# Kernel optimization log

Hardware: AMD Instinct MI355X
Metric: run time of the kernel (lower is better)

## Reference

```python
import jax, jax.numpy as jnp
import numpy as np

D_MODEL = 1024
N_HEADS = 16
D_HEAD = D_MODEL // N_HEADS


def _pid_proj(x, Wp, Wi, Wd, Wg, bg):
    # x: (B, T, D). PID decomposition: proportional / integral (running mean) / derivative (diff).
    T = x.shape[1]
    denom = jnp.arange(1, T + 1, dtype=x.dtype)[None, :, None]
    integral = jnp.cumsum(x, axis=1) / denom
    derivative = jnp.concatenate([jnp.zeros_like(x[:, :1]), x[:, 1:] - x[:, :-1]], axis=1)
    g = jax.nn.softmax(x @ Wg.T + bg, axis=-1)  # (B, T, 3)
    return (g[..., 0:1] * (x @ Wp.T)
            + g[..., 1:2] * (integral @ Wi.T)
            + g[..., 2:3] * (derivative @ Wd.T))


def setup_inputs() -> dict:
    key = jax.random.key(0)
    ks = jax.random.split(key, 16)
    B, T, D = 2, 2048, D_MODEL
    s = 1.0 / np.sqrt(D)

    def lin(k):
        return jax.random.uniform(k, (D, D), jnp.float32, -s, s)

    inp = {"x": jax.random.normal(ks[0], (B, T, D), jnp.float32)}
    names = ["q", "k", "v"]
    i = 1
    for n in names:
        inp[n + "Wp"] = lin(ks[i]); i += 1
        inp[n + "Wi"] = lin(ks[i]) * 0.1; i += 1
        inp[n + "Wd"] = lin(ks[i]) * 0.1; i += 1
        inp[n + "Wg"] = jax.random.uniform(ks[i], (3, D), jnp.float32, -s, s); i += 1
        inp[n + "bg"] = jnp.array([1.0, 0.0, 0.0], jnp.float32)
    inp["oW"] = lin(ks[i]); i += 1
    inp["ob"] = jax.random.uniform(ks[i], (D,), jnp.float32, -s, s)
    return inp


def reference(x, qWp, qWi, qWd, qWg, qbg,
              kWp, kWi, kWd, kWg, kbg,
              vWp, vWi, vWd, vWg, vbg, oW, ob):
    B, T, D = x.shape
    H, dh = N_HEADS, D_HEAD
    Q = _pid_proj(x, qWp, qWi, qWd, qWg, qbg).reshape(B, T, H, dh).transpose(0, 2, 1, 3)
    K = _pid_proj(x, kWp, kWi, kWd, kWg, kbg).reshape(B, T, H, dh).transpose(0, 2, 1, 3)
    V = _pid_proj(x, vWp, vWi, vWd, vWg, vbg).reshape(B, T, H, dh).transpose(0, 2, 1, 3)
    scale = jnp.sqrt(jnp.asarray(dh, x.dtype))
    scores = jnp.einsum('bhqd,bhkd->bhqk', Q, K) / scale  # (B,H,T,T)
    causal = jnp.triu(jnp.ones((T, T), bool), k=1)
    scores = jnp.where(causal[None, None], -jnp.inf, scores)
    attn = jax.nn.softmax(scores, axis=-1)
    out = jnp.einsum('bhqk,bhkd->bhqd', attn, V)
    out = out.transpose(0, 2, 1, 3).reshape(B, T, D)
    return out @ oW.T + ob
```

## Files before the change

kernel.cpp:

```cpp
#include <hip/hip_runtime.h>
#include <hip/hip_bf16.h>


#define D_MODEL 1024
#define T_SEQ   2048
#define B_SZ    2
#define M_ROWS  (B_SZ * T_SEQ)
#define N_HEADS 16
#define D_HEAD  64

typedef unsigned short u16;
typedef unsigned int   u32;

typedef short  short8  __attribute__((ext_vector_type(8)));
typedef float  float4v __attribute__((ext_vector_type(4)));

__device__ __forceinline__ float bf2f(u16 u) {
    union { u32 i; float f; } c; c.i = ((u32)u) << 16; return c.f;
}
__device__ __forceinline__ u16 f2bf(float f) {
    union { float f; u32 i; } c; c.f = f;
    u32 i = c.i;
    i += 0x7FFFu + ((i >> 16) & 1u);
    return (u16)(i >> 16);
}
__device__ __forceinline__ u16 f2bfc(float f) {
    __hip_bfloat16 h = __float2bfloat16(f);
    union { __hip_bfloat16 h; u16 u; } c; c.h = h; return c.u;
}
__device__ __forceinline__ float ldin(const void* p, int i, int fl) {
    return fl ? ((const float*)p)[i] : bf2f(((const u16*)p)[i]);
}

__global__ void detect_kernel(const u32* __restrict__ x, int* __restrict__ flag)
{
    if (threadIdx.x == 0 && blockIdx.x == 0) {
        int good = 0;
        for (int i = 0; i < 256; ++i) {
            union { u32 u; float f; } c; c.u = x[i];
            float a = fabsf(c.f);
            if (c.f == c.f && a > 1e-8f && a < 1e4f) ++good;
        }
        *flag = (good >= 192) ? 1 : 0;
    }
}

__global__ __launch_bounds__(256) void scan_partial(
    const void* __restrict__ x, float* __restrict__ csum,
    const int* __restrict__ flagp)
{
    int fl = *flagp;
    int tid = blockIdx.x * 256 + threadIdx.x;
    int b = tid >> 14;
    int c = (tid >> 10) & 15;
    int d = tid & 1023;
    int base = (b * T_SEQ + c * 128) * D_MODEL + d;
    float s = 0.f;
#pragma unroll 8
    for (int t = 0; t < 128; ++t) s += ldin(x, base + t * D_MODEL, fl);
    csum[tid] = s;
}

__global__ __launch_bounds__(256) void scan_final(
    const void* __restrict__ x, const float* __restrict__ csum,
    u16* __restrict__ integ, u16* __restrict__ db,
    const int* __restrict__ flagp)
{
    int fl = *flagp;
    int tid = blockIdx.x * 256 + threadIdx.x;
    int b = tid >> 14;
    int c = (tid >> 10) & 15;
    int d = tid & 1023;
    float pre = 0.f;
    int cbase = (b << 14) | d;
    for (int cc = 0; cc < c; ++cc) pre += csum[cbase + (cc << 10)];
    int base = (b * T_SEQ + c * 128) * D_MODEL + d;
    float run = pre;
    int t0 = c * 128;
    float xprev = (c != 0) ? ldin(x, base - D_MODEL, fl) : 0.f;
    for (int t = 0; t < 128; ++t) {
        float xv = ldin(x, base + t * D_MODEL, fl);
        run += xv;
        integ[base + t * D_MODEL] = f2bf(run / (float)(t0 + t + 1));
        float dv = (t0 + t == 0) ? 0.f : (xv - xprev);
        db[base + t * D_MODEL] = f2bf(dv);
        xprev = xv;
    }
}

__global__ __launch_bounds__(64) void gates_kernel(
    const void* __restrict__ x,
    const void* __restrict__ qWg, const void* __restrict__ qbg,
    const void* __restrict__ kWg, const void* __restrict__ kbg,
    const void* __restrict__ vWg, const void* __restrict__ vbg,
    float* __restrict__ gq, float* __restrict__ gk, float* __restrict__ gv,
    const int* __restrict__ flagp)
{
    int fl = *flagp;
    int row = blockIdx.x;
    int l = threadIdx.x;
    int xb = row * D_MODEL;
    float p[9];
#pragma unroll
    for (int j = 0; j < 9; ++j) p[j] = 0.f;
#pragma unroll 4
    for (int i = 0; i < 16; ++i) {
        int d = l + 64 * i;
        float xv = ldin(x, xb + d, fl);
        p[0] += xv * ldin(qWg, d, fl);
        p[1] += xv * ldin(qWg, 1024 + d, fl);
        p[2] += xv * ldin(qWg, 2048 + d, fl);
        p[3] += xv * ldin(kWg, d, fl);
        p[4] += xv * ldin(kWg, 1024 + d, fl);
        p[5] += xv * ldin(kWg, 2048 + d, fl);
        p[6] += xv * ldin(vWg, d, fl);
        p[7] += xv * ldin(vWg, 1024 + d, fl);
        p[8] += xv * ldin(vWg, 2048 + d, fl);
    }
#pragma unroll
    for (int off = 32; off > 0; off >>= 1) {
#pragma unroll
        for (int j = 0; j < 9; ++j) p[j] += __shfl_down(p[j], off);
    }
    if (l == 0) {
        const void* bgs[3] = { qbg, kbg, vbg };
        float* outs[3] = { gq, gk, gv };
#pragma unroll
        for (int pr = 0; pr < 3; ++pr) {
            float a0 = p[pr * 3 + 0] + ldin(bgs[pr], 0, fl);
            float a1 = p[pr * 3 + 1] + ldin(bgs[pr], 1, fl);
            float a2 = p[pr * 3 + 2] + ldin(bgs[pr], 2, fl);
            float mx = fmaxf(a0, fmaxf(a1, a2));
            float e0 = __expf(a0 - mx), e1 = __expf(a1 - mx), e2 = __expf(a2 - mx);
            float inv = 1.f / (e0 + e1 + e2);
            outs[pr][row * 3 + 0] = e0 * inv;
            outs[pr][row * 3 + 1] = e1 * inv;
            outs[pr][row * 3 + 2] = e2 * inv;
        }
    }
}

struct CvtArgs { const void* src[10]; };

__global__ __launch_bounds__(256) void cvt_w(
    CvtArgs a, u16* __restrict__ dst, const int* __restrict__ flagp)
{
    int fl = *flagp;
    int m = blockIdx.y;
    u16* d = dst + ((size_t)m << 20);
    int i = (blockIdx.x * 256 + threadIdx.x) * 8;
    if (fl) {
        const float* s = (const float*)a.src[m];
        float4 v0 = *(const float4*)(s + i);
        float4 v1 = *(const float4*)(s + i + 4);
        ushort4 o0, o1;
        o0.x = f2bfc(v0.x); o0.y = f2bfc(v0.y); o0.z = f2bfc(v0.z); o0.w = f2bfc(v0.w);
        o1.x = f2bfc(v1.x); o1.y = f2bfc(v1.y); o1.z = f2bfc(v1.z); o1.w = f2bfc(v1.w);
        *(ushort4*)(d + i) = o0;
        *(ushort4*)(d + i + 4) = o1;
    } else {
        const u16* s = (const u16*)a.src[m];
        *(ushort4*)(d + i)     = *(const ushort4*)(s + i);
        *(ushort4*)(d + i + 4) = *(const ushort4*)(s + i + 4);
    }
}

struct GemmArgs {
    const void* W[3][3];
    const float* G[3];
    u16* C[3];
};

template<int MODE, int BW16>
__global__ __launch_bounds__(256, 3) void mfma_gemm(
    const void* __restrict__ X, const u16* __restrict__ Ib,
    const u16* __restrict__ Abf, GemmArgs args,
    const void* __restrict__ bias, void* __restrict__ outp,
    const int* __restrict__ flagp, int Ktot)
{
    int fl = *flagp;
    __shared__ __align__(16) u16 As[2 * 4096];
    __shared__ __align__(16) u16 Bs[2 * 4096];

    int tid = threadIdx.x;
    int l = tid & 63, w = tid >> 6;
    int wm = w >> 1, wn = w & 1;
    int lin = blockIdx.x + (blockIdx.y << 3);
    int m0 = ((((lin & 7) << 2) + (lin >> 6))) * 128;
    int n0 = ((lin >> 3) & 7) * 128;
    int z = blockIdx.z;
    int lane15 = l & 15, quad = l >> 4;
    int srow = tid >> 2;
    int cs = tid & 3;
    int skof = cs * 8;

    const void* W0; const void* W1; const void* W2;
    const float* G = nullptr;
    u16* Chead = nullptr;
    if (MODE == 0) {
        W0 = args.W[z][0]; W1 = args.W[z][1]; W2 = args.W[z][2];
        G = args.G[z]; Chead = args.C[z];
    } else {
        W0 = args.W[0][0]; W1 = W0; W2 = W0;
    }

    float gcoef[2][3];
    if (MODE == 0) {
#pragma unroll
        for (int c = 0; c < 2; ++c)
#pragma unroll
            for (int s = 0; s < 3; ++s)
                gcoef[c][s] = G[(m0 + c * 64 + srow) * 3 + s];
    }

    ushort4 ra[2][2];
    ushort4 rb[2][2];

    auto cvt4 = [](float4 t) {
        ushort4 u;
        u.x = f2bfc(t.x); u.y = f2bfc(t.y); u.z = f2bfc(t.z); u.w = f2bfc(t.w);
        return u;
    };
    auto ld8 = [&](const void* p, int idx, ushort4& o0, ushort4& o1) {
        if (fl) {
            o0 = cvt4(*(const float4*)((const float*)p + idx));
            o1 = cvt4(*(const float4*)((const float*)p + idx + 4));
        } else {
            o0 = *(const ushort4*)((const u16*)p + idx);
            o1 = *(const ushort4*)((const u16*)p + idx + 4);
        }
    };

    auto load_phase = [&](int k0) {
        int seg = k0 >> 10, ksrc = k0 & 1023;
        const void* Wse = (MODE == 0) ? (seg == 0 ? W0 : (seg == 1 ? W1 : W2)) : W0;
#pragma unroll
        for (int c = 0; c < 2; ++c) {
            int gm = m0 + c * 64 + srow;
            int idx = gm * 1024 + ksrc + skof;
            if (MODE == 1) {
                ra[c][0] = *(const ushort4*)&Abf[idx];
                ra[c][1] = *(const ushort4*)&Abf[idx + 4];
            } else if (seg == 1) {
                ra[c][0] = *(const ushort4*)&Ib[idx];
                ra[c][1] = *(const ushort4*)&Ib[idx + 4];
            } else if (seg == 2) {
                ra[c][0] = *(const ushort4*)&Abf[idx];
                ra[c][1] = *(const ushort4*)&Abf[idx + 4];
            } else {
                ld8(X, idx, ra[c][0], ra[c][1]);
            }
            int gn = n0 + c * 64 + srow;
            int bidx = gn * 1024 + ksrc + skof;
            if (BW16) {
                const u16* bs = (const u16*)Wse;
                rb[c][0] = *(const ushort4*)&bs[bidx];
                rb[c][1] = *(const ushort4*)&bs[bidx + 4];
            } else {
                ld8(Wse, bidx, rb[c][0], rb[c][1]);
            }
        }
    };

    auto unp8 = [](ushort4 a, ushort4 b, float v[8]) {
        v[0] = bf2f(a.x); v[1] = bf2f(a.y); v[2] = bf2f(a.z); v[3] = bf2f(a.w);
        v[4] = bf2f(b.x); v[5] = bf2f(b.y); v[6] = bf2f(b.z); v[7] = bf2f(b.w);
    };

    int wo[2];
#pragma unroll
    for (int c = 0; c < 2; ++c) {
        int g = c * 16 + ((srow >> 4) << 2) + cs;
        wo[c] = (g << 7) | ((((srow & 15) + g) & 15) << 3);
    }

    auto store_phase = [&](int k0, int buf) {
        int seg = k0 >> 10;
        u16* Ad = As + buf * 4096;
        u16* Bd = Bs + buf * 4096;
#pragma unroll
        for (int c = 0; c < 2; ++c) {
            short8 pk;
            if (MODE == 1) {
                pk[0] = (short)ra[c][0].x; pk[1] = (short)ra[c][0].y;
                pk[2] = (short)ra[c][0].z; pk[3] = (short)ra[c][0].w;
                pk[4] = (short)ra[c][1].x; pk[5] = (short)ra[c][1].y;
                pk[6] = (short)ra[c][1].z; pk[7] = (short)ra[c][1].w;
            } else {
                float v[8];
                unp8(ra[c][0], ra[c][1], v);
                float sc = gcoef[c][seg];
#pragma unroll
                for (int j = 0; j < 8; ++j) pk[j] = (short)f2bfc(v[j] * sc);
            }
            *(short8*)&Ad[wo[c]] = pk;

            short8 pb;
            pb[0] = (short)rb[c][0].x; pb[1] = (short)rb[c][0].y;
            pb[2] = (short)rb[c][0].z; pb[3] = (short)rb[c][0].w;
            pb[4] = (short)rb[c][1].x; pb[5] = (short)rb[c][1].y;
            pb[6] = (short)rb[c][1].z; pb[7] = (short)rb[c][1].w;
            *(short8*)&Bd[wo[c]] = pb;
        }
    };

    float4v acc[4][4];
#pragma unroll
    for (int i = 0; i < 4; ++i)
#pragma unroll
        for (int j = 0; j < 4; ++j)
#pragma unroll
            for (int r = 0; r < 4; ++r) acc[i][j][r] = 0.f;

    int aro[4], bro[4];
#pragma unroll
    for (int t = 0; t < 4; ++t) {
        int ga = (wm * 4 + t) * 4 + quad;
        aro[t] = (ga << 7) | (((lane15 + ga) & 15) << 3);
        int gb = (wn * 4 + t) * 4 + quad;
        bro[t] = (gb << 7) | (((lane15 + gb) & 15) << 3);
    }

    int nIt = Ktot >> 5;
    load_phase(0);
    store_phase(0, 0);

    for (int it = 0; it < nIt; ++it) {
        __syncthreads();
        int cur = it & 1;
        if (it + 1 < nIt) load_phase((it + 1) << 5);

        short8 af[4], bfr[4];
#pragma unroll
        for (int ms = 0; ms < 4; ++ms)
            af[ms] = *(const short8*)&As[cur * 4096 + aro[ms]];
#pragma unroll
        for (int ns = 0; ns < 4; ++ns)
            bfr[ns] = *(const short8*)&Bs[cur * 4096 + bro[ns]];
#pragma unroll
        for (int ms = 0; ms < 4; ++ms)
#pragma unroll
            for (int ns = 0; ns < 4; ++ns)
                acc[ms][ns] = __builtin_amdgcn_mfma_f32_16x16x32_bf16(
                    af[ms], bfr[ns], acc[ms][ns], 0, 0, 0);

        if (it + 1 < nIt) store_phase((it + 1) << 5, 1 - cur);
    }

#pragma unroll
    for (int ms = 0; ms < 4; ++ms) {
#pragma unroll
        for (int r = 0; r < 4; ++r) {
            int m = m0 + wm * 64 + ms * 16 + quad * 4 + r;
#pragma unroll
            for (int ns = 0; ns < 4; ++ns) {
                int n = n0 + wn * 64 + ns * 16 + lane15;
                float vv = acc[ms][ns][r];
                if (MODE == 0) {
                    int b = m >> 11, t = m & (T_SEQ - 1);
                    int h = n >> 6,  d = n & 63;
                    Chead[(((b << 4) + h) * T_SEQ + t) * 64 + d] = f2bf(vv);
                } else {
                    vv += ldin(bias, n, fl);
                    if (fl) ((float*)outp)[m * 1024 + n] = vv;
                    else    ((u16*)outp)[m * 1024 + n] = f2bf(vv);
                }
            }
        }
    }
}

__global__ __launch_bounds__(256) void attn_mfma(
    const u16* __restrict__ Qh, const u16* __restrict__ Kh,
    const u16* __restrict__ Vh, u16* __restrict__ AO)
{
    int bx = blockIdx.x;
    int i  = bx & 31;
    int qt = (i & 1) ? (31 - (i >> 1)) : (i >> 1);
    int bh = bx >> 5;
    int h  = bh & 15;
    int b  = bh >> 4;
    int tid = threadIdx.x;
    int l   = tid & 63;
    int w   = tid >> 6;
    int lane15 = l & 15;
    int quad   = l >> 4;

    __shared__ __align__(16) u16 Ks[64 * 72];
    __shared__ __align__(16) u16 Vt[64 * 72];
    __shared__ __align__(16) u16 Ps[4 * 16 * 72];

    const u16* Qb = Qh + bh * (T_SEQ * 64);
    const u16* Kb = Kh + bh * (T_SEQ * 64);
    const u16* Vb = Vh + bh * (T_SEQ * 64);

    int qrow = qt * 64 + w * 16 + lane15;
    short8 qf[2];
#pragma unroll
    for (int ks = 0; ks < 2; ++ks)
        qf[ks] = *(const short8*)&Qb[qrow * 64 + ks * 32 + quad * 8];

    float4v oacc[4];
#pragma unroll
    for (int ds = 0; ds < 4; ++ds)
#pragma unroll
        for (int r = 0; r < 4; ++r) oacc[ds][r] = 0.f;
    float mrun[4], lrun[4];
#pragma unroll
    for (int r = 0; r < 4; ++r) { mrun[r] = -1e30f; lrun[r] = 0.f; }

    int srow = tid >> 2;
    int sdc  = (tid & 3) * 16;

    short8 kr0, kr1, vr0, vr1;
    auto load_regs = [&](int kt) {
        const u16* kp = &Kb[(kt * 64 + srow) * 64 + sdc];
        kr0 = *(const short8*)kp;
        kr1 = *(const short8*)(kp + 8);
        const u16* vp = &Vb[(kt * 64 + srow) * 64 + sdc];
        vr0 = *(const short8*)vp;
        vr1 = *(const short8*)(vp + 8);
    };
    auto store_lds = [&]() {
        *(short8*)&Ks[srow * 72 + sdc] = kr0;
        *(short8*)&Ks[srow * 72 + sdc + 8] = kr1;
        u16 vv[16];
        *(short8*)&vv[0] = vr0;
        *(short8*)&vv[8] = vr1;
#pragma unroll
        for (int e2 = 0; e2 < 16; ++e2)
            Vt[(sdc + e2) * 72 + srow] = vv[e2];
    };

    load_regs(0);

    for (int kt = 0; kt <= qt; ++kt) {
        store_lds();
        __syncthreads();
        if (kt < qt) load_regs(kt + 1);

        float4v sacc[4];
#pragma unroll
        for (int ns = 0; ns < 4; ++ns)
#pragma unroll
            for (int r = 0; r < 4; ++r) sacc[ns][r] = 0.f;
#pragma unroll
        for (int ks = 0; ks < 2; ++ks) {
#pragma unroll
            for (int ns = 0; ns < 4; ++ns) {
                short8 bfk = *(const short8*)&Ks[(ns * 16 + lane15) * 72 + ks * 32 + quad * 8];
                sacc[ns] = __builtin_amdgcn_mfma_f32_16x16x32_bf16(
                    qf[ks], bfk, sacc[ns], 0, 0, 0);
            }
        }

        if (kt == qt) {
            int qg0 = qt * 64 + w * 16 + quad * 4;
#pragma unroll
            for (int ns = 0; ns < 4; ++ns) {
                int kg = kt * 64 + ns * 16 + lane15;
#pragma unroll
                for (int r = 0; r < 4; ++r) {
                    float s = sacc[ns][r] * 0.125f;
                    sacc[ns][r] = (kg > qg0 + r) ? -1e30f : s;
                }
            }
        } else {
#pragma unroll
            for (int ns = 0; ns < 4; ++ns)
#pragma unroll
                for (int r = 0; r < 4; ++r)
                    sacc[ns][r] *= 0.125f;
        }

#pragma unroll
        for (int r = 0; r < 4; ++r) {
            float mx = fmaxf(fmaxf(sacc[0][r], sacc[1][r]),
                             fmaxf(sacc[2][r], sacc[3][r]));
#pragma unroll
            for (int m2 = 1; m2 < 16; m2 <<= 1)
                mx = fmaxf(mx, __shfl_xor(mx, m2, 64));
            float mnew = fmaxf(mrun[r], mx);
            float al = __expf(mrun[r] - mnew);
            float rs = 0.f;
#pragma unroll
            for (int ns = 0; ns < 4; ++ns) {
                float p = __expf(sacc[ns][r] - mnew);
                sacc[ns][r] = p;
                rs += p;
            }
#pragma unroll
            for (int m2 = 1; m2 < 16; m2 <<= 1)
                rs += __shfl_xor(rs, m2, 64);
            lrun[r] = lrun[r] * al + rs;
            mrun[r] = mnew;
#pragma unroll
            for (int ds = 0; ds < 4; ++ds) oacc[ds][r] *= al;
        }

        u16* Pw = &Ps[w * 16 * 72];
#pragma unroll
        for (int ns = 0; ns < 4; ++ns)
#pragma unroll
            for (int r = 0; r < 4; ++r)
                Pw[(quad * 4 + r) * 72 + ns * 16 + lane15] = f2bf(sacc[ns][r]);

#pragma unroll
        for (int ks = 0; ks < 2; ++ks) {
            short8 afp = *(const short8*)&Pw[lane15 * 72 + ks * 32 + quad * 8];
#pragma unroll
            for (int ds = 0; ds < 4; ++ds) {
                short8 bfv = *(const short8*)&Vt[(ds * 16 + lane15) * 72 + ks * 32 + quad * 8];
                oacc[ds] = __builtin_amdgcn_mfma_f32_16x16x32_bf16(
                    afp, bfv, oacc[ds], 0, 0, 0);
            }
        }
        __syncthreads();
    }

#pragma unroll
    for (int r = 0; r < 4; ++r) {
        float inv = 1.f / lrun[r];
        int t = qt * 64 + w * 16 + quad * 4 + r;
        int orow = (b * T_SEQ + t) * 1024 + h * 64;
#pragma unroll
        for (int ds = 0; ds < 4; ++ds)
            AO[orow + ds * 16 + lane15] = f2bf(oacc[ds][r] * inv);
    }
}

extern "C" void kernel_launch(void* const* d_in, const int* in_sizes, int n_in,
                              void* d_out, int out_size, void* d_ws, size_t ws_size,
                              hipStream_t stream)
{
    const void* x   = d_in[0];
    const void* qWp = d_in[1];
    const void* qWi = d_in[2];
    const void* qWd = d_in[3];
    const void* qWg = d_in[4];
    const void* qbg = d_in[5];
    const void* kWp = d_in[6];
    const void* kWi = d_in[7];
    const void* kWd = d_in[8];
    const void* kWg = d_in[9];
    const void* kbg = d_in[10];
    const void* vWp = d_in[11];
    const void* vWi = d_in[12];
    const void* vWd = d_in[13];
    const void* vWg = d_in[14];
    const void* vbg = d_in[15];
    const void* oW  = d_in[16];
    const void* ob  = d_in[17];

    const size_t SZ = (size_t)M_ROWS * D_MODEL;

    int*   flag = (int*)d_ws;
    float* fws  = (float*)d_ws;
    float* csum = fws + 64;
    float* gq   = csum + 32768;
    float* gk   = gq + 3 * M_ROWS;
    float* gv   = gk + 3 * M_ROWS;
    u16* Ib = (u16*)((char*)d_ws + (1u << 20));
    u16* AO = Ib;
    u16* Qh = Ib + SZ;
    u16* Kh = Qh + SZ;
    u16* Vh = Kh + SZ;

    u16* db = (u16*)d_out;

    const size_t NEED_FULL = (size_t)(1u << 20) + 4 * SZ * 2 + ((size_t)10 << 21);
    u16* wb = (ws_size >= NEED_FULL) ? (Vh + SZ) : nullptr;

    detect_kernel<<<1, 64, 0, stream>>>((const u32*)x, flag);
    scan_partial<<<128, 256, 0, stream>>>(x, csum, flag);
    scan_final<<<128, 256, 0, stream>>>(x, csum, Ib, db, flag);
    gates_kernel<<<M_ROWS, 64, 0, stream>>>(x, qWg, qbg, kWg, kbg, vWg, vbg,
                                            gq, gk, gv, flag);

    GemmArgs pa;
    pa.G[0] = gq; pa.G[1] = gk; pa.G[2] = gv;
    pa.C[0] = Qh; pa.C[1] = Kh; pa.C[2] = Vh;
    GemmArgs oa = {};

    if (wb) {
        CvtArgs ca;
        ca.src[0] = qWp; ca.src[1] = qWi; ca.src[2] = qWd;
        ca.src[3] = kWp; ca.src[4] = kWi; ca.src[5] = kWd;
        ca.src[6] = vWp; ca.src[7] = vWi; ca.src[8] = vWd;
        ca.src[9] = oW;
        cvt_w<<<dim3(512, 10), 256, 0, stream>>>(ca, wb, flag);

        for (int z2 = 0; z2 < 3; ++z2)
            for (int s2 = 0; s2 < 3; ++s2)
                pa.W[z2][s2] = wb + ((size_t)(z2 * 3 + s2) << 20);
        oa.W[0][0] = wb + ((size_t)9 << 20);

        mfma_gemm<0, 1><<<dim3(8, 32, 3), 256, 0, stream>>>(
            x, Ib, db, pa, nullptr, nullptr, flag, 3072);
        attn_mfma<<<B_SZ * N_HEADS * (T_SEQ / 64), 256, 0, stream>>>(Qh, Kh, Vh, AO);
        mfma_gemm<1, 1><<<dim3(8, 32, 1), 256, 0, stream>>>(
            nullptr, nullptr, AO, oa, ob, d_out, flag, 1024);
    } else {
        pa.W[0][0] = qWp; pa.W[0][1] = qWi; pa.W[0][2] = qWd;
        pa.W[1][0] = kWp; pa.W[1][1] = kWi; pa.W[1][2] = kWd;
        pa.W[2][0] = vWp; pa.W[2][1] = vWi; pa.W[2][2] = vWd;
        oa.W[0][0] = oW;

        mfma_gemm<0, 0><<<dim3(8, 32, 3), 256, 0, stream>>>(
            x, Ib, db, pa, nullptr, nullptr, flag, 3072);
        attn_mfma<<<B_SZ * N_HEADS * (T_SEQ / 64), 256, 0, stream>>>(Qh, Kh, Vh, AO);
        mfma_gemm<1, 0><<<dim3(8, 32, 1), 256, 0, stream>>>(
            nullptr, nullptr, AO, oa, ob, d_out, flag, 1024);
    }
}
```

Baseline: 494.0 us.

## Split-K the output projection with atomics and double scan chunk count

The output projection GEMM is split along K into two halves. Each half atomically adds into an fp32 accumulator that is zeroed first, and a separate kernel then adds the bias and writes the output, doubling the block count on a grid that previously had only 256 blocks. The prefix-scan kernels now use 64-row chunks instead of 128-row chunks, giving twice as many threads and a shorter serial loop per thread. This adds a memset, atomic traffic and an extra launch in exchange for better CU occupancy.

```diff
diff --git a/kernel.cpp b/kernel.cpp
--- a/kernel.cpp
+++ b/kernel.cpp
@@ -51,13 +51,13 @@
 {
     int fl = *flagp;
     int tid = blockIdx.x * 256 + threadIdx.x;
-    int b = tid >> 14;
-    int c = (tid >> 10) & 15;
+    int b = tid >> 15;
+    int c = (tid >> 10) & 31;
     int d = tid & 1023;
-    int base = (b * T_SEQ + c * 128) * D_MODEL + d;
+    int base = (b * T_SEQ + c * 64) * D_MODEL + d;
     float s = 0.f;
 #pragma unroll 8
-    for (int t = 0; t < 128; ++t) s += ldin(x, base + t * D_MODEL, fl);
+    for (int t = 0; t < 64; ++t) s += ldin(x, base + t * D_MODEL, fl);
     csum[tid] = s;
 }
 
@@ -68,17 +68,17 @@
 {
     int fl = *flagp;
     int tid = blockIdx.x * 256 + threadIdx.x;
-    int b = tid >> 14;
-    int c = (tid >> 10) & 15;
+    int b = tid >> 15;
+    int c = (tid >> 10) & 31;
     int d = tid & 1023;
     float pre = 0.f;
-    int cbase = (b << 14) | d;
+    int cbase = (b << 15) | d;
     for (int cc = 0; cc < c; ++cc) pre += csum[cbase + (cc << 10)];
-    int base = (b * T_SEQ + c * 128) * D_MODEL + d;
+    int base = (b * T_SEQ + c * 64) * D_MODEL + d;
     float run = pre;
-    int t0 = c * 128;
+    int t0 = c * 64;
     float xprev = (c != 0) ? ldin(x, base - D_MODEL, fl) : 0.f;
-    for (int t = 0; t < 128; ++t) {
+    for (int t = 0; t < 64; ++t) {
         float xv = ldin(x, base + t * D_MODEL, fl);
         run += xv;
         integ[base + t * D_MODEL] = f2bf(run / (float)(t0 + t + 1));
@@ -165,13 +165,34 @@
     }
 }
 
+__global__ __launch_bounds__(256) void finish_o(
+    const float* __restrict__ acc32, const void* __restrict__ bias,
+    void* __restrict__ outp, const int* __restrict__ flagp)
+{
+    int fl = *flagp;
+    int i4 = (blockIdx.x * 256 + threadIdx.x) * 4;
+    float4 v = *(const float4*)(acc32 + i4);
+    int n = i4 & 1023;
+    v.x += ldin(bias, n + 0, fl);
+    v.y += ldin(bias, n + 1, fl);
+    v.z += ldin(bias, n + 2, fl);
+    v.w += ldin(bias, n + 3, fl);
+    if (fl) {
+        *(float4*)((float*)outp + i4) = v;
+    } else {
+        ushort4 o;
+        o.x = f2bfc(v.x); o.y = f2bfc(v.y); o.z = f2bfc(v.z); o.w = f2bfc(v.w);
+        *(ushort4*)((u16*)outp + i4) = o;
+    }
+}
+
 struct GemmArgs {
     const void* W[3][3];
     const float* G[3];
     u16* C[3];
 };
 
-template<int MODE, int BW16>
+template<int MODE, int BW16, int SPLIT>
 __global__ __launch_bounds__(256, 3) void mfma_gemm(
     const void* __restrict__ X, const u16* __restrict__ Ib,
     const u16* __restrict__ Abf, GemmArgs args,
@@ -189,6 +210,7 @@
     int m0 = ((((lin & 7) << 2) + (lin >> 6))) * 128;
     int n0 = ((lin >> 3) & 7) * 128;
     int z = blockIdx.z;
+    int kbase = (MODE == 1 && SPLIT) ? (z << 9) : 0;
     int lane15 = l & 15, quad = l >> 4;
     int srow = tid >> 2;
     int cs = tid & 3;
@@ -232,7 +254,7 @@
     };
 
     auto load_phase = [&](int k0) {
-        int seg = k0 >> 10, ksrc = k0 & 1023;
+        int seg = k0 >> 10, ksrc = (k0 & 1023) + kbase;
         const void* Wse = (MODE == 0) ? (seg == 0 ? W0 : (seg == 1 ? W1 : W2)) : W0;
 #pragma unroll
         for (int c = 0; c < 2; ++c) {
@@ -360,6 +382,8 @@
                     int b = m >> 11, t = m & (T_SEQ - 1);
                     int h = n >> 6,  d = n & 63;
                     Chead[(((b << 4) + h) * T_SEQ + t) * 64 + d] = f2bf(vv);
+                } else if (SPLIT) {
+                    atomicAdd(&((float*)outp)[m * 1024 + n], vv);
                 } else {
                     vv += ldin(bias, n, fl);
                     if (fl) ((float*)outp)[m * 1024 + n] = vv;
@@ -557,7 +581,7 @@
     int*   flag = (int*)d_ws;
     float* fws  = (float*)d_ws;
     float* csum = fws + 64;
-    float* gq   = csum + 32768;
+    float* gq   = csum + 65536;
     float* gk   = gq + 3 * M_ROWS;
     float* gv   = gk + 3 * M_ROWS;
     u16* Ib = (u16*)((char*)d_ws + (1u << 20));
@@ -567,13 +591,14 @@
     u16* Vh = Kh + SZ;
 
     u16* db = (u16*)d_out;
+    float* acc32 = (float*)Qh;
 
     const size_t NEED_FULL = (size_t)(1u << 20) + 4 * SZ * 2 + ((size_t)10 << 21);
     u16* wb = (ws_size >= NEED_FULL) ? (Vh + SZ) : nullptr;
 
     detect_kernel<<<1, 64, 0, stream>>>((const u32*)x, flag);
-    scan_partial<<<128, 256, 0, stream>>>(x, csum, flag);
-    scan_final<<<128, 256, 0, stream>>>(x, csum, Ib, db, flag);
+    scan_partial<<<256, 256, 0, stream>>>(x, csum, flag);
+    scan_final<<<256, 256, 0, stream>>>(x, csum, Ib, db, flag);
     gates_kernel<<<M_ROWS, 64, 0, stream>>>(x, qWg, qbg, kWg, kbg, vWg, vbg,
                                             gq, gk, gv, flag);
 
@@ -595,21 +620,24 @@
                 pa.W[z2][s2] = wb + ((size_t)(z2 * 3 + s2) << 20);
         oa.W[0][0] = wb + ((size_t)9 << 20);
 
-        mfma_gemm<0, 1><<<dim3(8, 32, 3), 256, 0, stream>>>(
+        mfma_gemm<0, 1, 0><<<dim3(8, 32, 3), 256, 0, stream>>>(
             x, Ib, db, pa, nullptr, nullptr, flag, 3072);
         attn_mfma<<<B_SZ * N_HEADS * (T_SEQ / 64), 256, 0, stream>>>(Qh, Kh, Vh, AO);
-        mfma_gemm<1, 1><<<dim3(8, 32, 1), 256, 0, stream>>>(
-            nullptr, nullptr, AO, oa, ob, d_out, flag, 1024);
+
+        hipMemsetAsync(acc32, 0, SZ * sizeof(float), stream);
+        mfma_gemm<1, 1, 1><<<dim3(8, 32, 2), 256, 0, stream>>>(
+            nullptr, nullptr, AO, oa, nullptr, acc32, flag, 512);
+        finish_o<<<4096, 256, 0, stream>>>(acc32, ob, d_out, flag);
     } else {
         pa.W[0][0] = qWp; pa.W[0][1] = qWi; pa.W[0][2] = qWd;
         pa.W[1][0] = kWp; pa.W[1][1] = kWi; pa.W[1][2] = kWd;
         pa.W[2][0] = vWp; pa.W[2][1] = vWi; pa.W[2][2] = vWd;
         oa.W[0][0] = oW;
 
-        mfma_gemm<0, 0><<<dim3(8, 32, 3), 256, 0, stream>>>(
+        mfma_gemm<0, 0, 0><<<dim3(8, 32, 3), 256, 0, stream>>>(
             x, Ib, db, pa, nullptr, nullptr, flag, 3072);
         attn_mfma<<<B_SZ * N_HEADS * (T_SEQ / 64), 256, 0, stream>>>(Qh, Kh, Vh, AO);
-        mfma_gemm<1, 0><<<dim3(8, 32, 1), 256, 0, stream>>>(
+        mfma_gemm<1, 0, 0><<<dim3(8, 32, 1), 256, 0, stream>>>(
             nullptr, nullptr, AO, oa, ob, d_out, flag, 1024);
     }
 }
```

Measured after the change: 1.053 ms. 113% more time.
